# Optimization experiments

Hardware: AMD Instinct MI355X
Metric: run time of the kernel (lower is better)

The kernel has to match this reference:

```python
import jax, jax.numpy as jnp
import numpy as np

B, T = 128, 512
V, E, U, K = 50000, 100, 128, 32


def _lstm(x, Wk, Wr, b):
    # x: [B, T, D] -> [B, T, U], Keras LSTM gate order i,f,g,o
    Bd = x.shape[0]
    Ud = Wr.shape[0]
    xs = jnp.swapaxes(x, 0, 1)  # [T, B, D]

    def step(carry, xt):
        h, c = carry
        z = xt @ Wk + h @ Wr + b
        i, f, g, o = jnp.split(z, 4, axis=-1)
        c = jax.nn.sigmoid(f) * c + jax.nn.sigmoid(i) * jnp.tanh(g)
        h = jax.nn.sigmoid(o) * jnp.tanh(c)
        return (h, c), h

    init = (jnp.zeros((Bd, Ud), x.dtype), jnp.zeros((Bd, Ud), x.dtype))
    _, hs = jax.lax.scan(step, init, xs)
    return jnp.swapaxes(hs, 0, 1)


def _crf_logZ(em, trans):
    # em: [B, T, K] emissions; trans: [K, K]. Forward algorithm log-partition.
    alpha0 = em[:, 0]  # [B, K]
    es = jnp.swapaxes(em[:, 1:], 0, 1)  # [T-1, B, K]

    def step(alpha, et):
        # alpha[b, i] + trans[i, j] -> logsumexp over i, plus emission
        alpha = jax.nn.logsumexp(alpha[:, :, None] + trans[None], axis=1) + et
        return alpha, None

    alphaT, _ = jax.lax.scan(step, alpha0, es)
    return jax.nn.logsumexp(alphaT, axis=-1)  # [B]


def setup_inputs() -> dict:
    key = jax.random.key(0)
    ks = jax.random.split(key, 11)
    s = 0.1
    return {
        "tokens": jax.random.randint(ks[0], (B, T), 0, V, dtype=jnp.int32),
        "emb": jax.random.normal(ks[1], (V, E), jnp.float32) * s,
        "Wk_f": jax.random.normal(ks[2], (E, 4 * U), jnp.float32) * s,
        "Wr_f": jax.random.normal(ks[3], (U, 4 * U), jnp.float32) * s,
        "b_f": jnp.zeros((4 * U,), jnp.float32),
        "Wk_b": jax.random.normal(ks[4], (E, 4 * U), jnp.float32) * s,
        "Wr_b": jax.random.normal(ks[5], (U, 4 * U), jnp.float32) * s,
        "b_b": jnp.zeros((4 * U,), jnp.float32),
        "crf_kernel": jax.random.normal(ks[6], (2 * U, K), jnp.float32) * s,
        "crf_bias": jnp.zeros((K,), jnp.float32),
        "trans": jax.random.normal(ks[7], (K, K), jnp.float32) * s,
    }


def reference(tokens, emb, Wk_f, Wr_f, b_f, Wk_b, Wr_b, b_b, crf_kernel, crf_bias, trans):
    x = emb[tokens]  # [B, T, E]
    h_f = _lstm(x, Wk_f, Wr_f, b_f)
    h_b = _lstm(x[:, ::-1], Wk_b, Wr_b, b_b)[:, ::-1]
    h = jnp.concatenate([h_f, h_b], axis=-1)  # [B, T, 2U] (dropout = identity at inference)
    em = h @ crf_kernel + crf_bias  # [B, T, K] CRF emission potentials
    return _crf_logZ(em, trans)  # [B] log-partition via CRF forward DP
```

## Files before the change

### kernel.cpp

```cpp
#include <hip/hip_runtime.h>
#include <hip/hip_bf16.h>

#define B_  128
#define T_  512
#define V_  50000
#define VP  50016
#define E_  100
#define U_  128
#define K_  32
#define G4  512
#define KP  128

typedef _Float16 h2_t __attribute__((ext_vector_type(2)));
typedef _Float16 f16x8 __attribute__((ext_vector_type(8)));
typedef __fp16   h2raw_t __attribute__((ext_vector_type(2)));
typedef short    bf16x8 __attribute__((ext_vector_type(8)));
typedef float    f32x4  __attribute__((ext_vector_type(4)));

#define LGKM_BARRIER() do {                                   \
    asm volatile("s_waitcnt lgkmcnt(0)" ::: "memory");        \
    __builtin_amdgcn_s_barrier();                             \
    asm volatile("" ::: "memory");                            \
} while (0)

__device__ __forceinline__ h2_t pk2(float a, float b) {
    h2raw_t r = __builtin_amdgcn_cvt_pkrtz(a, b);
    union { h2raw_t r; h2_t h; } u; u.r = r; return u.h;
}

#if __has_builtin(__builtin_amdgcn_rcpf)
__device__ __forceinline__ float rcp_f(float x) { return __builtin_amdgcn_rcpf(x); }
#else
__device__ __forceinline__ float rcp_f(float x) { return 1.f / x; }
#endif

__device__ __forceinline__ unsigned short bf16_bits(float v) {
    __hip_bfloat16 b = __float2bfloat16(v);
    union { __hip_bfloat16 b; unsigned short s; } u; u.b = b; return u.s;
}
__device__ __forceinline__ float bf2f(unsigned short u) {
    union { unsigned int i; float f; } x; x.i = ((unsigned int)u) << 16; return x.f;
}

__global__ __launch_bounds__(128) void pack_b_kernel(
    const float* __restrict__ Wk_f, const float* __restrict__ Wk_b,
    __hip_bfloat16* __restrict__ Bb)
{
    const int n = blockIdx.x;
    const int k = threadIdx.x;
    float v = 0.f;
    if (k < E_) v = (n < 512) ? Wk_f[k * 512 + n] : Wk_b[k * 512 + (n - 512)];
    Bb[n * KP + k] = __float2bfloat16(v);
}

__global__ __launch_bounds__(512, 1) void proj_mfma_kernel(
    const float* __restrict__ emb,
    const __hip_bfloat16* __restrict__ Bb,
    const float* __restrict__ b_f, const float* __restrict__ b_b,
    __hip_bfloat16* __restrict__ proj)
{
    const int r0   = blockIdx.x * 64;
    const int tid  = threadIdx.x;
    const int wv   = tid >> 6;
    const int lane = tid & 63;
    const int quad = lane >> 4;
    const int l16  = lane & 15;
    const int mh   = wv >> 2;
    const int cg   = wv & 3;

    __shared__ __align__(16) float C_lds[64][268];
    unsigned short* A_st = (unsigned short*)&C_lds[0][0];

    for (int idx = tid; idx < 64 * 64; idx += 512) {
        int r = idx >> 6, kk = idx & 63;
        int vr = r0 + r; if (vr >= V_) vr = V_ - 1;
        unsigned int w = 0;
        if (kk < 50) {
            float2 v = *(const float2*)(emb + (long long)vr * E_ + 2 * kk);
            w = ((unsigned int)bf16_bits(v.y) << 16) | bf16_bits(v.x);
        }
        *(unsigned int*)&A_st[r * 136 + 2 * kk] = w;
    }
    LGKM_BARRIER();

    bf16x8 af[2][4];
    #pragma unroll
    for (int mt = 0; mt < 2; ++mt)
        #pragma unroll
        for (int kc = 0; kc < 4; ++kc)
            af[mt][kc] = *(const bf16x8*)&A_st[(mh * 32 + mt * 16 + l16) * 136 +
                                               kc * 32 + quad * 8];
    LGKM_BARRIER();

    const unsigned short* Bu = (const unsigned short*)Bb;

    for (int ng = 0; ng < 4; ++ng) {
        const int n0 = ng * 256;

        bf16x8 bfr[4][4];
        #pragma unroll
        for (int nt = 0; nt < 4; ++nt)
            #pragma unroll
            for (int kc = 0; kc < 4; ++kc)
                bfr[nt][kc] = *(const bf16x8*)(Bu +
                    (n0 + cg * 64 + nt * 16 + l16) * KP + kc * 32 + quad * 8);

        f32x4 acc[2][4];
        #pragma unroll
        for (int mt = 0; mt < 2; ++mt)
            #pragma unroll
            for (int nt = 0; nt < 4; ++nt)
                acc[mt][nt] = (f32x4){0.f, 0.f, 0.f, 0.f};

        #pragma unroll
        for (int mt = 0; mt < 2; ++mt)
            #pragma unroll
            for (int nt = 0; nt < 4; ++nt)
                #pragma unroll
                for (int kc = 0; kc < 4; ++kc)
                    acc[mt][nt] = __builtin_amdgcn_mfma_f32_16x16x32_bf16(
                        af[mt][kc], bfr[nt][kc], acc[mt][nt], 0, 0, 0);

        #pragma unroll
        for (int mt = 0; mt < 2; ++mt)
            #pragma unroll
            for (int nt = 0; nt < 4; ++nt)
                #pragma unroll
                for (int v = 0; v < 4; ++v)
                    C_lds[mh * 32 + mt * 16 + quad * 4 + v]
                         [cg * 64 + nt * 16 + l16] = acc[mt][nt][v];
        LGKM_BARRIER();

        const float* bias = (n0 < 512) ? b_f : b_b;
        const int nbase = n0 & 511;
        for (int idx = tid; idx < 64 * 128; idx += 512) {
            int r = idx >> 7, cc = (idx & 127) * 2;
            float v0 = C_lds[r][cc]     + bias[nbase + cc];
            float v1 = C_lds[r][cc + 1] + bias[nbase + cc + 1];
            unsigned int w = ((unsigned int)bf16_bits(v1) << 16) | bf16_bits(v0);
            int row = r0 + r; if (row >= VP) row = VP - 1;
            *(unsigned int*)(proj + (long long)row * 1024 + n0 + cc) = w;
        }
        LGKM_BARRIER();
    }
}

__device__ __forceinline__ float sigmoid_f(float x) {
    return rcp_f(1.f + __expf(-x));
}
__device__ __forceinline__ float tanh_f(float x) {
    return 1.f - 2.f * rcp_f(__expf(2.f * x) + 1.f);
}

__global__ __launch_bounds__(512, 1) void lstm_kernel(
    const __hip_bfloat16* __restrict__ proj,
    const int* __restrict__ tokens,
    const float* __restrict__ Wr_f, const float* __restrict__ Wr_b,
    __hip_bfloat16* __restrict__ h_buf)
{
    const int bid  = blockIdx.x;
    const int dir  = bid >> 5;
    const int b0   = (bid & 31) * 4;
    const int tid  = threadIdx.x;
    const int w    = tid >> 6;
    const int lane = tid & 63;
    const int quad = lane >> 4;
    const int l16  = lane & 15;
    const int unit = 16 * w + l16;

    const float* Wr = dir ? Wr_b : Wr_f;

    union uf16 { f16x8 v; h2_t p[4]; };
    f16x8 wb[4][4];
    #pragma unroll
    for (int gq = 0; gq < 4; ++gq) {
        const int col = gq * 128 + unit;
        #pragma unroll
        for (int kc = 0; kc < 4; ++kc) {
            const int k0 = kc * 32 + quad * 8;
            uf16 u;
            #pragma unroll
            for (int jj = 0; jj < 4; ++jj)
                u.p[jj] = pk2(Wr[(k0 + 2 * jj)     * G4 + col],
                              Wr[(k0 + 2 * jj + 1) * G4 + col]);
            wb[gq][kc] = u.v;
        }
    }

    __shared__ __align__(16) _Float16      h_lds[2][4][144];
    __shared__ __align__(16) unsigned short xkb[2][4][520];
    __shared__ unsigned short tok_lds[4][512];

    for (int idx = tid; idx < 4 * 512; idx += 512) {
        int chain = idx >> 9, tt = idx & 511;
        int tsrc = dir ? (T_ - 1 - tt) : tt;
        tok_lds[chain][tt] = (unsigned short)tokens[(b0 + chain) * T_ + tsrc];
    }
    for (int idx = tid; idx < 4 * 144; idx += 512)
        ((_Float16*)h_lds[0])[idx] = (_Float16)0.f;
    __syncthreads();

    const int sc = tid >> 7;
    const int sj = tid & 127;
    const unsigned short* prbase = (const unsigned short*)proj + dir * 512;

    int v[4][2];
    #pragma unroll
    for (int d = 0; d < 4; ++d) {
        int tk = tok_lds[sc][d];
        const unsigned int* p32 = (const unsigned int*)(prbase + (size_t)tk * 1024);
        v[d][0] = p32[sj];
        v[d][1] = p32[sj + 128];
    }
    *(unsigned int*)&xkb[0][sc][2 * sj]       = v[0][0];
    *(unsigned int*)&xkb[0][sc][2 * sj + 256] = v[0][1];
    __syncthreads();

    float c = 0.f;

    for (int t4 = 0; t4 < T_ / 4; ++t4) {
        #pragma unroll
        for (int u = 0; u < 4; ++u) {
            const int t  = t4 * 4 + u;
            const int cb = u & 1, nb = cb ^ 1;

            f16x8 a[4];
            #pragma unroll
            for (int kc = 0; kc < 4; ++kc)
                a[kc] = *(const f16x8*)&h_lds[cb][l16 >> 2][kc * 32 + quad * 8];
            unsigned short xk[4];
            #pragma unroll
            for (int gq = 0; gq < 4; ++gq)
                xk[gq] = xkb[cb][quad][gq * 128 + unit];

            {
                int tnx = t + 4; if (tnx > T_ - 1) tnx = T_ - 1;
                int tk = tok_lds[sc][tnx];
                const unsigned int* p32 =
                    (const unsigned int*)(prbase + (size_t)tk * 1024);
                v[u][0] = p32[sj];
                v[u][1] = p32[sj + 128];
            }

            f32x4 acc[4];
            #pragma unroll
            for (int gq = 0; gq < 4; ++gq)
                acc[gq] = (f32x4){0.f, 0.f, 0.f, 0.f};
            #pragma unroll
            for (int gq = 0; gq < 4; ++gq)
                #pragma unroll
                for (int kc = 0; kc < 4; ++kc)
                    acc[gq] = __builtin_amdgcn_mfma_f32_16x16x32_f16(
                        a[kc], wb[gq][kc], acc[gq], 0, 0, 0);

            float zi = acc[0][0] + bf2f(xk[0]);
            float zf = acc[1][0] + bf2f(xk[1]);
            float zg = acc[2][0] + bf2f(xk[2]);
            float zo = acc[3][0] + bf2f(xk[3]);
            c = sigmoid_f(zf) * c + sigmoid_f(zi) * tanh_f(zg);
            float h = sigmoid_f(zo) * tanh_f(c);
            h_lds[nb][quad][unit] = (_Float16)h;

            const int ttime = dir ? (T_ - 1 - t) : t;
            h_buf[((size_t)(b0 + quad) * T_ + ttime) * 256 + dir * 128 + unit] =
                __float2bfloat16(h);

            {
                const int pw = (u + 1) & 3;
                *(unsigned int*)&xkb[nb][sc][2 * sj]       = v[pw][0];
                *(unsigned int*)&xkb[nb][sc][2 * sj + 256] = v[pw][1];
            }

            LGKM_BARRIER();
        }
    }
}

__global__ __launch_bounds__(256) void em_kernel(
    const __hip_bfloat16* __restrict__ h_buf,
    const float* __restrict__ ck, const float* __restrict__ cb,
    float* __restrict__ em)
{
    const int tid  = threadIdx.x;
    const int part = tid >> 5;
    const int k    = tid & 31;

    float ckr[32];
    #pragma unroll
    for (int i = 0; i < 32; ++i)
        ckr[i] = ck[(part * 32 + i) * K_ + k];
    const float cbk = cb[k];

    __shared__ float h_l[8][256];
    __shared__ float part_l[8][8][K_];

    const int r0 = blockIdx.x * 64;

    for (int round = 0; round < 8; ++round) {
        const int rbase = r0 + round * 8;
        #pragma unroll
        for (int j = 0; j < 8; ++j)
            h_l[j][tid] = __bfloat162float(h_buf[(long long)(rbase + j) * 256 + tid]);
        LGKM_BARRIER();

        #pragma unroll
        for (int j = 0; j < 8; ++j) {
            float pp = 0.f;
            #pragma unroll
            for (int i = 0; i < 32; ++i)
                pp = fmaf(h_l[j][part * 32 + i], ckr[i], pp);
            part_l[j][part][k] = pp;
        }
        LGKM_BARRIER();

        {
            int j2 = tid >> 5;
            float e = cbk;
            #pragma unroll
            for (int pq = 0; pq < 8; ++pq) e += part_l[j2][pq][k];
            em[(long long)(rbase + j2) * K_ + k] = e;
        }
        LGKM_BARRIER();
    }
}

#define PF_ 8
__global__ __launch_bounds__(64) void crf_kernel(
    const float* __restrict__ em,
    const float* __restrict__ trans,
    float* __restrict__ out)
{
    const int b    = blockIdx.x;
    const int lane = threadIdx.x;
    const int k    = lane & 31;
    const int half = lane >> 5;

    float etr[16];
    #pragma unroll
    for (int i = 0; i < 16; ++i)
        etr[i] = __expf(trans[(half * 16 + i) * K_ + k]);

    const float* em_b = em + (long long)b * T_ * K_;

    float ep[PF_];
    #pragma unroll
    for (int d = 0; d < PF_; ++d)
        ep[d] = em_b[d * K_ + k];

    float w = 0.f;
    float L = 0.f;
    for (int tb = 0; tb < T_; tb += PF_) {
        float en[PF_];
        if (tb + PF_ < T_) {
            #pragma unroll
            for (int d = 0; d < PF_; ++d)
                en[d] = em_b[(tb + PF_ + d) * K_ + k];
        } else {
            #pragma unroll
            for (int d = 0; d < PF_; ++d) en[d] = 0.f;
        }

        float eem[PF_];
        #pragma unroll
        for (int d = 0; d < PF_; ++d) eem[d] = __expf(ep[d]);

        #pragma unroll
        for (int d = 0; d < PF_; ++d) {
            if (tb + d == 0) {
                w = eem[d];
            } else {
                float a0 = 0.f, a1 = 0.f, a2 = 0.f, a3 = 0.f;
                #pragma unroll
                for (int i = 0; i < 4; ++i)
                    a0 = fmaf(__shfl(w, half * 16 + i,      64), etr[i],      a0);
                #pragma unroll
                for (int i = 0; i < 4; ++i)
                    a1 = fmaf(__shfl(w, half * 16 + 4 + i,  64), etr[4 + i],  a1);
                #pragma unroll
                for (int i = 0; i < 4; ++i)
                    a2 = fmaf(__shfl(w, half * 16 + 8 + i,  64), etr[8 + i],  a2);
                #pragma unroll
                for (int i = 0; i < 4; ++i)
                    a3 = fmaf(__shfl(w, half * 16 + 12 + i, 64), etr[12 + i], a3);
                float acc = (a0 + a1) + (a2 + a3);
                acc += __shfl_xor(acc, 32, 64);
                w = acc * eem[d];
            }
        }

        {
            float w0 = __shfl(w, 0, 64);
            w *= rcp_f(w0);
            L += __logf(w0);
        }

        #pragma unroll
        for (int d = 0; d < PF_; ++d) ep[d] = en[d];
    }

    float s = w;
    #pragma unroll
    for (int d = 1; d < 32; d <<= 1)
        s += __shfl_xor(s, d, 64);
    if (lane == 0) out[b] = L + __logf(s);
}

extern "C" void kernel_launch(void* const* d_in, const int* in_sizes, int n_in,
                              void* d_out, int out_size, void* d_ws, size_t ws_size,
                              hipStream_t stream)
{
    const int*   tokens = (const int*)  d_in[0];
    const float* emb    = (const float*)d_in[1];
    const float* Wk_f   = (const float*)d_in[2];
    const float* Wr_f   = (const float*)d_in[3];
    const float* b_f    = (const float*)d_in[4];
    const float* Wk_b   = (const float*)d_in[5];
    const float* Wr_b   = (const float*)d_in[6];
    const float* b_b    = (const float*)d_in[7];
    const float* ck     = (const float*)d_in[8];
    const float* cb     = (const float*)d_in[9];
    const float* trans  = (const float*)d_in[10];
    float* out = (float*)d_out;

    const long long ROWS = (long long)B_ * T_;
    __hip_bfloat16* proj  = (__hip_bfloat16*)d_ws;
    __hip_bfloat16* h_buf = proj + (long long)VP * 1024;
    float* em = (float*)(h_buf + ROWS * 256);
    __hip_bfloat16* Bb = (__hip_bfloat16*)(em + ROWS * K_);

    hipLaunchKernelGGL(pack_b_kernel, dim3(1024), dim3(128), 0, stream,
                       Wk_f, Wk_b, Bb);
    hipLaunchKernelGGL(proj_mfma_kernel, dim3((VP + 63) / 64), dim3(512), 0, stream,
                       emb, Bb, b_f, b_b, proj);
    hipLaunchKernelGGL(lstm_kernel, dim3(64), dim3(512), 0, stream,
                       proj, tokens, Wr_f, Wr_b, h_buf);
    hipLaunchKernelGGL(em_kernel, dim3((int)(ROWS / 64)), dim3(256), 0, stream,
                       h_buf, ck, cb, em);
    hipLaunchKernelGGL(crf_kernel, dim3(B_), dim3(64), 0, stream,
                       em, trans, out);
}
```

Measured before the change: 522.6 us.

## Fuse CRF emission projection into LSTM kernel via per-direction MFMA partials

Removes the separate emission kernel and the bf16 hidden-state buffer. Each LSTM block keeps 8 ring-buffered hidden states in LDS and, every 4 steps, two waves compute that direction's half of the emission projection with MFMA. The results are written to per-direction emission buffers, which the CRF kernel sums and then adds the bias. This avoids a global round-trip of the hidden states and one launch. In exchange it adds work and LDS reads inside the latency-bound recurrent loop, and emissions are now computed with fp16 inputs.

```diff
diff --git a/kernel.cpp b/kernel.cpp
--- a/kernel.cpp
+++ b/kernel.cpp
@@ -156,7 +156,8 @@
     const __hip_bfloat16* __restrict__ proj,
     const int* __restrict__ tokens,
     const float* __restrict__ Wr_f, const float* __restrict__ Wr_b,
-    __hip_bfloat16* __restrict__ h_buf)
+    const float* __restrict__ ck,
+    float* __restrict__ em_f, float* __restrict__ em_bw)
 {
     const int bid  = blockIdx.x;
     const int dir  = bid >> 5;
@@ -169,6 +170,7 @@
     const int unit = 16 * w + l16;
 
     const float* Wr = dir ? Wr_b : Wr_f;
+    float* eout = dir ? em_bw : em_f;
 
     union uf16 { f16x8 v; h2_t p[4]; };
     f16x8 wb[4][4];
@@ -187,7 +189,21 @@
         }
     }
 
-    __shared__ __align__(16) _Float16      h_lds[2][4][144];
+    f16x8 ckb[4];
+    if (w < 2) {
+        #pragma unroll
+        for (int kc = 0; kc < 4; ++kc) {
+            const int k0 = dir * 128 + kc * 32 + quad * 8;
+            uf16 u;
+            #pragma unroll
+            for (int jj = 0; jj < 4; ++jj)
+                u.p[jj] = pk2(ck[(k0 + 2 * jj)     * K_ + w * 16 + l16],
+                              ck[(k0 + 2 * jj + 1) * K_ + w * 16 + l16]);
+            ckb[kc] = u.v;
+        }
+    }
+
+    __shared__ __align__(16) _Float16      h_lds[8][4][144];
     __shared__ __align__(16) unsigned short xkb[2][4][520];
     __shared__ unsigned short tok_lds[4][512];
 
@@ -223,11 +239,13 @@
         for (int u = 0; u < 4; ++u) {
             const int t  = t4 * 4 + u;
             const int cb = u & 1, nb = cb ^ 1;
+            const int hr = t & 7;
+            const int hw = (t + 1) & 7;
 
             f16x8 a[4];
             #pragma unroll
             for (int kc = 0; kc < 4; ++kc)
-                a[kc] = *(const f16x8*)&h_lds[cb][l16 >> 2][kc * 32 + quad * 8];
+                a[kc] = *(const f16x8*)&h_lds[hr][l16 >> 2][kc * 32 + quad * 8];
             unsigned short xk[4];
             #pragma unroll
             for (int gq = 0; gq < 4; ++gq)
@@ -259,11 +277,7 @@
             float zo = acc[3][0] + bf2f(xk[3]);
             c = sigmoid_f(zf) * c + sigmoid_f(zi) * tanh_f(zg);
             float h = sigmoid_f(zo) * tanh_f(c);
-            h_lds[nb][quad][unit] = (_Float16)h;
-
-            const int ttime = dir ? (T_ - 1 - t) : t;
-            h_buf[((size_t)(b0 + quad) * T_ + ttime) * 256 + dir * 128 + unit] =
-                __float2bfloat16(h);
+            h_lds[hw][quad][unit] = (_Float16)h;
 
             {
                 const int pw = (u + 1) & 3;
@@ -273,60 +287,35 @@
 
             LGKM_BARRIER();
         }
-    }
-}
-
-__global__ __launch_bounds__(256) void em_kernel(
-    const __hip_bfloat16* __restrict__ h_buf,
-    const float* __restrict__ ck, const float* __restrict__ cb,
-    float* __restrict__ em)
-{
-    const int tid  = threadIdx.x;
-    const int part = tid >> 5;
-    const int k    = tid & 31;
-
-    float ckr[32];
-    #pragma unroll
-    for (int i = 0; i < 32; ++i)
-        ckr[i] = ck[(part * 32 + i) * K_ + k];
-    const float cbk = cb[k];
-
-    __shared__ float h_l[8][256];
-    __shared__ float part_l[8][8][K_];
-
-    const int r0 = blockIdx.x * 64;
-
-    for (int round = 0; round < 8; ++round) {
-        const int rbase = r0 + round * 8;
-        #pragma unroll
-        for (int j = 0; j < 8; ++j)
-            h_l[j][tid] = __bfloat162float(h_buf[(long long)(rbase + j) * 256 + tid]);
-        LGKM_BARRIER();
-
-        #pragma unroll
-        for (int j = 0; j < 8; ++j) {
-            float pp = 0.f;
-            #pragma unroll
-            for (int i = 0; i < 32; ++i)
-                pp = fmaf(h_l[j][part * 32 + i], ckr[i], pp);
-            part_l[j][part][k] = pp;
-        }
-        LGKM_BARRIER();
-
-        {
-            int j2 = tid >> 5;
-            float e = cbk;
-            #pragma unroll
-            for (int pq = 0; pq < 8; ++pq) e += part_l[j2][pq][k];
-            em[(long long)(rbase + j2) * K_ + k] = e;
-        }
-        LGKM_BARRIER();
+
+        if (w < 2) {
+            const int base = (t4 & 1) * 4 + 1;
+            const int d    = l16 >> 2;
+            const int ch   = l16 & 3;
+            const int rbuf = (base + d) & 7;
+            f16x8 ea[4];
+            #pragma unroll
+            for (int kc = 0; kc < 4; ++kc)
+                ea[kc] = *(const f16x8*)&h_lds[rbuf][ch][kc * 32 + quad * 8];
+            f32x4 e = (f32x4){0.f, 0.f, 0.f, 0.f};
+            #pragma unroll
+            for (int kc = 0; kc < 4; ++kc)
+                e = __builtin_amdgcn_mfma_f32_16x16x32_f16(
+                    ea[kc], ckb[kc], e, 0, 0, 0);
+            const int step = t4 * 4 + quad;
+            const int tte  = dir ? (T_ - 1 - step) : step;
+            #pragma unroll
+            for (int vv = 0; vv < 4; ++vv)
+                eout[((size_t)(b0 + vv) * T_ + tte) * K_ + (w << 4) + l16] =
+                    e[vv];
+        }
     }
 }
 
 #define PF_ 8
 __global__ __launch_bounds__(64) void crf_kernel(
-    const float* __restrict__ em,
+    const float* __restrict__ em_f, const float* __restrict__ em_bw,
+    const float* __restrict__ cb,
     const float* __restrict__ trans,
     float* __restrict__ out)
 {
@@ -340,12 +329,14 @@
     for (int i = 0; i < 16; ++i)
         etr[i] = __expf(trans[(half * 16 + i) * K_ + k]);
 
-    const float* em_b = em + (long long)b * T_ * K_;
+    const float cbk = cb[k];
+    const float* ef = em_f  + (long long)b * T_ * K_;
+    const float* eb = em_bw + (long long)b * T_ * K_;
 
     float ep[PF_];
     #pragma unroll
     for (int d = 0; d < PF_; ++d)
-        ep[d] = em_b[d * K_ + k];
+        ep[d] = ef[d * K_ + k] + eb[d * K_ + k] + cbk;
 
     float w = 0.f;
     float L = 0.f;
@@ -354,7 +345,8 @@
         if (tb + PF_ < T_) {
             #pragma unroll
             for (int d = 0; d < PF_; ++d)
-                en[d] = em_b[(tb + PF_ + d) * K_ + k];
+                en[d] = ef[(tb + PF_ + d) * K_ + k] +
+                        eb[(tb + PF_ + d) * K_ + k] + cbk;
         } else {
             #pragma unroll
             for (int d = 0; d < PF_; ++d) en[d] = 0.f;
@@ -423,19 +415,17 @@
     float* out = (float*)d_out;
 
     const long long ROWS = (long long)B_ * T_;
-    __hip_bfloat16* proj  = (__hip_bfloat16*)d_ws;
-    __hip_bfloat16* h_buf = proj + (long long)VP * 1024;
-    float* em = (float*)(h_buf + ROWS * 256);
-    __hip_bfloat16* Bb = (__hip_bfloat16*)(em + ROWS * K_);
+    __hip_bfloat16* proj = (__hip_bfloat16*)d_ws;
+    float* em_f  = (float*)(proj + (long long)VP * 1024);
+    float* em_bw = em_f + ROWS * K_;
+    __hip_bfloat16* Bb = (__hip_bfloat16*)(em_bw + ROWS * K_);
 
     hipLaunchKernelGGL(pack_b_kernel, dim3(1024), dim3(128), 0, stream,
                        Wk_f, Wk_b, Bb);
     hipLaunchKernelGGL(proj_mfma_kernel, dim3((VP + 63) / 64), dim3(512), 0, stream,
                        emb, Bb, b_f, b_b, proj);
     hipLaunchKernelGGL(lstm_kernel, dim3(64), dim3(512), 0, stream,
-                       proj, tokens, Wr_f, Wr_b, h_buf);
-    hipLaunchKernelGGL(em_kernel, dim3((int)(ROWS / 64)), dim3(256), 0, stream,
-                       h_buf, ck, cb, em);
+                       proj, tokens, Wr_f, Wr_b, ck, em_f, em_bw);
     hipLaunchKernelGGL(crf_kernel, dim3(B_), dim3(64), 0, stream,
-                       em, trans, out);
-}
+                       em_f, em_bw, cb, trans, out);
+}
```

Result: no change. 519.8 us (-0.5%).
